# Kernel optimization log

Hardware: AMD Instinct MI355X
Metric: run time of the kernel (lower is better)

## Reference

```python
import jax, jax.numpy as jnp
import numpy as np

H, L, OUT = 128, 3, 128
N, E, NRG, ERG, M, G = 200_000, 600_000, 100_000, 300_000, 200_000, 10_000
BN_EPS = 1e-5


def setup_inputs() -> dict:
    key = jax.random.key(0)
    ks = iter(jax.random.split(key, 32))
    rint = lambda shape, hi: jax.random.randint(next(ks), shape, 0, hi, dtype=jnp.int64 if False else jnp.int32)
    inp = {
        "node_feat": rint((N, 9), 100),
        "edge_index": rint((2, E), N),
        "edge_feat": rint((E, 3), 100),
        "batch": jnp.sort(rint((N,), G)),
        "mapping_row": rint((M,), N),
        "mapping_col": rint((M,), NRG),
        "rg_edge_index": rint((2, ERG), NRG),
        "rg_atom_features": rint((NRG,), 8),
        "tree_batch": jnp.sort(rint((NRG,), G)),
        "num_graphs": G,
    }
    s = 0.05
    nrm = lambda shape: jax.random.normal(next(ks), shape, dtype=jnp.float32) * s
    inp.update({
        "atom_emb": nrm((9, 100, H)),
        "bond_emb": nrm((L, 3, 100, H)),
        "rg_emb": nrm((8, H)),
        "atom_W1": nrm((L, H, 2 * H)),
        "atom_W2": nrm((L, 2 * H, H)),
        "rg_W1": nrm((L, H, 2 * H)),
        "rg_W2": nrm((L, 2 * H, H)),
        "raw2rg_W": nrm((L, H, H)),
        "rg2raw_W": nrm((L, H, H)),
        "atom_lin_W": nrm((H, H)),
        "rg_lin_W": nrm((H, H)),
        "lin_W": nrm((H, OUT)),
    })
    return inp


def _scatter_mean(src, idx, n):
    s = jax.ops.segment_sum(src, idx, num_segments=n)
    c = jax.ops.segment_sum(jnp.ones((src.shape[0], 1), src.dtype), idx, num_segments=n)
    return s / jnp.maximum(c, 1.0)


def _bn(h):  # BatchNorm1d(affine=False), batch statistics
    mu = h.mean(0)
    var = h.var(0)
    return (h - mu) * jax.lax.rsqrt(var + BN_EPS)


def _gin_mlp(h, W1, W2):  # Linear -> BN -> ReLU -> Linear (all bias-free)
    return jax.nn.relu(_bn(h @ W1)) @ W2


def reference(node_feat, edge_index, edge_feat, batch, mapping_row, mapping_col,
              rg_edge_index, rg_atom_features, tree_batch, num_graphs,
              atom_emb, bond_emb, rg_emb, atom_W1, atom_W2, rg_W1, rg_W2,
              raw2rg_W, rg2raw_W, atom_lin_W, rg_lin_W, lin_W):
    n = node_feat.shape[0]
    n_rg = rg_atom_features.shape[0]
    src, dst = edge_index[0], edge_index[1]
    rsrc, rdst = rg_edge_index[0], rg_edge_index[1]

    # AtomEncoder: sum of 9 embedding lookups -> [n, H]
    x = atom_emb[jnp.arange(9), node_feat].sum(axis=1)
    rg = rg_emb[rg_atom_features]  # [n_rg, H]

    for i in range(L):
        # BondEncoder + GINEConv: sum_j relu(x_j + e_ij) aggregated at dst
        e = bond_emb[i][jnp.arange(3), edge_feat].sum(axis=1)  # [E, H]
        agg = jax.ops.segment_sum(jax.nn.relu(x[src] + e), dst, num_segments=n)
        x = jax.nn.relu(_bn(_gin_mlp(x + agg, atom_W1[i], atom_W2[i])))

        # raw -> reduced-graph inter message passing (scatter mean over mapping)
        rg = rg + jax.nn.relu(_scatter_mean(x[mapping_row], mapping_col, n_rg) @ raw2rg_W[i])

        # GINConv on reduced graph
        agg_rg = jax.ops.segment_sum(rg[rsrc], rdst, num_segments=n_rg)
        rg = jax.nn.relu(_bn(_gin_mlp(rg + agg_rg, rg_W1[i], rg_W2[i])))

        # reduced-graph -> raw inter message passing
        x = x + jax.nn.relu(_scatter_mean(rg[mapping_col], mapping_row, n) @ rg2raw_W[i])

    # graph-level readout (mean pooling)
    xg = _scatter_mean(x, batch, num_graphs) @ atom_lin_W
    rgg = _scatter_mean(rg, tree_batch, num_graphs) @ rg_lin_W
    return jax.nn.relu(xg + rgg) @ lin_W  # [num_graphs, OUT]
```

## Files before the change

kernel.cpp:

```cpp
#include <hip/hip_runtime.h>
#include <hip/hip_bf16.h>
#include <cstdint>
#include <cstddef>

#define H 128

using f32x4v = __attribute__((ext_vector_type(4))) float;
using bf8 = __attribute__((ext_vector_type(8))) short;

__device__ __forceinline__ short f2bf(float f) {
  unsigned u = __float_as_uint(f);
  u = (u + 0x7fffu + ((u >> 16) & 1u)) >> 16;
  return (short)u;
}
__device__ __forceinline__ float bf2f(short h) {
  return __uint_as_float(((unsigned)(unsigned short)h) << 16);
}
__device__ __forceinline__ void splitf(float f, short& h, short& l) {
  h = f2bf(f);
  l = f2bf(f - bf2f(h));
}
__device__ __forceinline__ f32x4v mfma16(bf8 a, bf8 b, f32x4v c) {
  return __builtin_amdgcn_mfma_f32_16x16x32_bf16(a, b, c, 0, 0, 0);
}

__device__ __forceinline__ void load_afrags(const float* __restrict__ Ap, bool av,
    float sc, bf8* ah, bf8* al_) {
#pragma unroll
  for (int ks = 0; ks < 4; ++ks) {
    float v[8];
    if (av) {
      f32x4v p0 = *(const f32x4v*)(Ap + ks * 32);
      f32x4v p1 = *(const f32x4v*)(Ap + ks * 32 + 4);
      v[0]=p0.x*sc; v[1]=p0.y*sc; v[2]=p0.z*sc; v[3]=p0.w*sc;
      v[4]=p1.x*sc; v[5]=p1.y*sc; v[6]=p1.z*sc; v[7]=p1.w*sc;
    } else {
#pragma unroll
      for (int j = 0; j < 8; ++j) v[j] = 0.f;
    }
#pragma unroll
    for (int j = 0; j < 8; ++j) { short hh, ll; splitf(v[j], hh, ll); ah[ks][j]=hh; al_[ks][j]=ll; }
  }
}


__global__ __launch_bounds__(256) void pack_w_k(const float* __restrict__ W,
    short* __restrict__ hi, short* __restrict__ lo, int K, int N) {
  int total = K * N;
  int t = blockIdx.x * 256 + threadIdx.x;
  int layer = blockIdx.y;
  if (t >= total) return;
  int k = t / N, n = t - k * N;
  float f = W[(size_t)layer * total + t];
  short h, l; splitf(f, h, l);
  int nt = n >> 4, ks = k >> 5, kk = k & 31;
  int lane = (n & 15) | (((kk >> 3) & 3) << 4);
  size_t idx = (size_t)layer * total + ((size_t)(nt * (K >> 5) + ks) << 9) + lane * 8 + (kk & 7);
  hi[idx] = h; lo[idx] = l;
}


__global__ __launch_bounds__(256) void atom_encode_k(const int* __restrict__ nf,
    const float* __restrict__ emb, float* __restrict__ x, int N) {
  long long t = (long long)blockIdx.x * 256 + threadIdx.x;
  if (t >= (long long)N * H) return;
  int n = (int)(t >> 7), h = (int)(t & 127);
  const int* row = nf + (size_t)n * 9;
  float s = 0.f;
#pragma unroll
  for (int f = 0; f < 9; ++f) s += emb[((size_t)f * 100 + row[f]) * H + h];
  x[t] = s;
}

__global__ __launch_bounds__(256) void rg_init_k(const int* __restrict__ feat,
    const float* __restrict__ emb, float* __restrict__ rg, int NRG) {
  long long t = (long long)blockIdx.x * 256 + threadIdx.x;
  if (t >= (long long)NRG * H) return;
  int n = (int)(t >> 7), h = (int)(t & 127);
  rg[t] = emb[(size_t)feat[n] * H + h];
}


__global__ __launch_bounds__(256) void icount_k(const int* __restrict__ idx,
    int* __restrict__ cnt, int n) {
  int t = blockIdx.x * 256 + threadIdx.x;
  if (t < n) atomicAdd(&cnt[idx[t]], 1);
}

__global__ __launch_bounds__(256) void inv_from_int_k(const int* __restrict__ c,
    float* __restrict__ inv, int n) {
  int t = blockIdx.x * 256 + threadIdx.x;
  if (t < n) inv[t] = 1.0f / (float)max(c[t], 1);
}

__global__ __launch_bounds__(256) void seg_blocksum_k(const int* __restrict__ cnt,
    int* __restrict__ bsum, int n) {
  __shared__ int red[256];
  int base = blockIdx.x * 1024;
  int s = 0;
  for (int i = threadIdx.x; i < 1024; i += 256) {
    int idx = base + i;
    s += (idx < n) ? cnt[idx] : 0;
  }
  red[threadIdx.x] = s; __syncthreads();
  for (int st = 128; st > 0; st >>= 1) {
    if (threadIdx.x < st) red[threadIdx.x] += red[threadIdx.x + st];
    __syncthreads();
  }
  if (threadIdx.x == 0) bsum[blockIdx.x] = red[0];
}

__global__ __launch_bounds__(256) void seg_scan_k(const int* __restrict__ cnt,
    const int* __restrict__ bsum, int* __restrict__ off, int* __restrict__ cur,
    int n, int nblk) {
  __shared__ int pref;
  __shared__ int tsum[257];
  int b = blockIdx.x;
  if (threadIdx.x == 0) {
    int p = 0;
    for (int j = 0; j < b; ++j) p += bsum[j];
    pref = p;
  }
  int base = b * 1024 + threadIdx.x * 4;
  int v[4]; int s = 0;
#pragma unroll
  for (int j = 0; j < 4; ++j) { int idx = base + j; v[j] = (idx < n) ? cnt[idx] : 0; s += v[j]; }
  tsum[threadIdx.x + 1] = s;
  if (threadIdx.x == 0) tsum[0] = 0;
  __syncthreads();
  if (threadIdx.x == 0) { for (int j = 1; j <= 256; ++j) tsum[j] += tsum[j - 1]; }
  __syncthreads();
  int run = pref + tsum[threadIdx.x];
#pragma unroll
  for (int j = 0; j < 4; ++j) {
    int idx = base + j;
    if (idx < n) { off[idx] = run; cur[idx] = run; }
    run += v[j];
  }
  if (b == 0 && threadIdx.x == 0) {
    int tot = 0;
    for (int j = 0; j < nblk; ++j) tot += bsum[j];
    off[n] = tot;
  }
}

__global__ __launch_bounds__(256) void seg_fill_k(const int* __restrict__ idx,
    int* __restrict__ cur, int* __restrict__ ids, int n) {
  int t = blockIdx.x * 256 + threadIdx.x;
  if (t < n) { int p = atomicAdd(&cur[idx[t]], 1); ids[p] = t; }
}


__global__ __launch_bounds__(256) void gine_agg_k(const int* __restrict__ off,
    const int* __restrict__ ids, const int* __restrict__ ei, const int* __restrict__ ef,
    const float* __restrict__ bemb, const float* __restrict__ x,
    float* __restrict__ out, int N) {
  int n = blockIdx.x * 8 + (threadIdx.x >> 5);
  if (n >= N) return;
  int c4 = (threadIdx.x & 31) * 4;
  float4 acc = *(const float4*)(x + (size_t)n * H + c4);
  int p0 = off[n], p1 = off[n + 1];
  for (int p = p0; p < p1; ++p) {
    int e = ids[p];
    int src = ei[e];
    const int* f = ef + (size_t)e * 3;
    float4 v0 = *(const float4*)(bemb + (size_t)f[0] * H + c4);
    float4 v1 = *(const float4*)(bemb + ((size_t)100 + f[1]) * H + c4);
    float4 v2 = *(const float4*)(bemb + ((size_t)200 + f[2]) * H + c4);
    float4 xs = *(const float4*)(x + (size_t)src * H + c4);
    acc.x += fmaxf(xs.x + v0.x + v1.x + v2.x, 0.f);
    acc.y += fmaxf(xs.y + v0.y + v1.y + v2.y, 0.f);
    acc.z += fmaxf(xs.z + v0.z + v1.z + v2.z, 0.f);
    acc.w += fmaxf(xs.w + v0.w + v1.w + v2.w, 0.f);
  }
  *(float4*)(out + (size_t)n * H + c4) = acc;
}

__global__ __launch_bounds__(256) void gather_agg_k(const int* __restrict__ off,
    const int* __restrict__ ids, const int* __restrict__ sidx,
    const float* __restrict__ src, const float* __restrict__ base,
    float* __restrict__ out, int N) {
  int n = blockIdx.x * 8 + (threadIdx.x >> 5);
  if (n >= N) return;
  int c4 = (threadIdx.x & 31) * 4;
  float4 acc = make_float4(0.f, 0.f, 0.f, 0.f);
  if (base) acc = *(const float4*)(base + (size_t)n * H + c4);
  int p0 = off[n], p1 = off[n + 1];
  for (int p = p0; p < p1; ++p) {
    int m = ids[p];
    int sr = sidx ? sidx[m] : m;
    float4 v = *(const float4*)(src + (size_t)sr * H + c4);
    acc.x += v.x; acc.y += v.y; acc.z += v.z; acc.w += v.w;
  }
  *(float4*)(out + (size_t)n * H + c4) = acc;
}

__device__ __forceinline__ int lowb(const int* __restrict__ a, int n, int v) {
  int lo = 0, hi = n;
  while (lo < hi) { int mid = (lo + hi) >> 1; if (a[mid] < v) lo = mid + 1; else hi = mid; }
  return lo;
}

__global__ __launch_bounds__(256) void pool_mean_k(const int* __restrict__ bidx,
    const float* __restrict__ src, float* __restrict__ out, int n, int G) {
  int g = blockIdx.x * 8 + (threadIdx.x >> 5);
  if (g >= G) return;
  int c4 = (threadIdx.x & 31) * 4;
  int lo = lowb(bidx, n, g), hi = lowb(bidx, n, g + 1);
  float4 acc = make_float4(0.f, 0.f, 0.f, 0.f);
  for (int r = lo; r < hi; ++r) {
    float4 v = *(const float4*)(src + (size_t)r * H + c4);
    acc.x += v.x; acc.y += v.y; acc.z += v.z; acc.w += v.w;
  }
  float inv = 1.0f / (float)max(hi - lo, 1);
  acc.x *= inv; acc.y *= inv; acc.z *= inv; acc.w *= inv;
  *(float4*)(out + (size_t)g * H + c4) = acc;
}


__global__ void bn_final_k(const float* __restrict__ ssum, const float* __restrict__ ssq,
    float* __restrict__ mu, float* __restrict__ rsig, int C, float invM) {
  int c = threadIdx.x + blockIdx.x * blockDim.x;
  if (c < C) {
    float m = ssum[c] * invM;
    float v = ssq[c] * invM - m * m;
    mu[c] = m;
    rsig[c] = rsqrtf(v + 1e-5f);
  }
}

__global__ __launch_bounds__(256) void bn_apply_relu_k(const float* __restrict__ X,
    const float* __restrict__ mu, const float* __restrict__ rsig,
    float* __restrict__ Out, int M) {
  long long t = (long long)blockIdx.x * 256 + threadIdx.x;
  if (t >= (long long)M * 32) return;
  int c4 = ((int)(t & 31)) * 4;
  float4 v = ((const float4*)X)[t];
  float4 m4 = *(const float4*)&mu[c4];
  float4 r4 = *(const float4*)&rsig[c4];
  v.x = fmaxf((v.x - m4.x) * r4.x, 0.f);
  v.y = fmaxf((v.y - m4.y) * r4.y, 0.f);
  v.z = fmaxf((v.z - m4.z) * r4.z, 0.f);
  v.w = fmaxf((v.w - m4.w) * r4.w, 0.f);
  ((float4*)Out)[t] = v;
}


__global__ __launch_bounds__(512) void mlp_stats_mfma_k(
    const float* __restrict__ A, const short* __restrict__ w1h, const short* __restrict__ w1l,
    float* __restrict__ ssum, float* __restrict__ ssq, int M, int npairs) {
  __shared__ __align__(16) short Wch[8192], Wcl[8192];
  __shared__ float sRed[256], qRed[256];
  int tid = threadIdx.x;
  if (tid < 256) { sRed[tid] = 0.f; qRed[tid] = 0.f; }
  int w = tid >> 6, l = tid & 63, l15 = l & 15, lg = l >> 4;
  int h = w >> 2, wl = w & 3;
  float sAcc[16], qAcc[16];
#pragma unroll
  for (int nt = 0; nt < 16; ++nt) { sAcc[nt] = 0.f; qAcc[nt] = 0.f; }
  for (int pb = blockIdx.x; pb < npairs; pb += gridDim.x) {
    int tile = pb * 2 + h;
    int arow = tile * 64 + wl * 16 + l15;
    bool av = arow < M;
    bf8 ah[4], al_[4];
    load_afrags(A + (size_t)arow * 128 + lg * 8, av, 1.f, ah, al_);
    for (int ch = 0; ch < 4; ++ch) {
      __syncthreads();
      const bf8* srcH = (const bf8*)(w1h + ch * 8192);
      const bf8* srcL = (const bf8*)(w1l + ch * 8192);
      for (int it = tid; it < 1024; it += 512) {
        ((bf8*)Wch)[it] = srcH[it];
        ((bf8*)Wcl)[it] = srcL[it];
      }
      __syncthreads();
#pragma unroll
      for (int ntl = 0; ntl < 4; ++ntl) {
        f32x4v c = {0.f, 0.f, 0.f, 0.f};
#pragma unroll
        for (int ks = 0; ks < 4; ++ks) {
          bf8 bh = *(const bf8*)&Wch[(ntl * 4 + ks) * 512 + l * 8];
          bf8 bl = *(const bf8*)&Wcl[(ntl * 4 + ks) * 512 + l * 8];
          c = mfma16(al_[ks], bh, c);
          c = mfma16(ah[ks], bl, c);
          c = mfma16(ah[ks], bh, c);
        }
        int nt = ch * 4 + ntl;
        if (av) {
          sAcc[nt] += c[0] + c[1] + c[2] + c[3];
          qAcc[nt] += c[0]*c[0] + c[1]*c[1] + c[2]*c[2] + c[3]*c[3];
        }
      }
    }
  }
  __syncthreads();
#pragma unroll
  for (int nt = 0; nt < 16; ++nt) {
    float s = sAcc[nt], q = qAcc[nt];
    s += __shfl_xor(s, 16); s += __shfl_xor(s, 32);
    q += __shfl_xor(q, 16); q += __shfl_xor(q, 32);
    if (l < 16) { atomicAdd(&sRed[nt * 16 + l], s); atomicAdd(&qRed[nt * 16 + l], q); }
  }
  __syncthreads();
  if (tid < 256) { atomicAdd(&ssum[tid], sRed[tid]); atomicAdd(&ssq[tid], qRed[tid]); }
}



__global__ __launch_bounds__(512) void mlp_fused_mfma_k(
    float* __restrict__ A, const short* __restrict__ w1h, const short* __restrict__ w1l,
    const short* __restrict__ w2h, const short* __restrict__ w2l,
    const float* __restrict__ mu, const float* __restrict__ rsig,
    float* __restrict__ ssum, float* __restrict__ ssq, int M, int npairs) {
  __shared__ __align__(16) short Wch[8192], Wcl[8192];
  __shared__ __align__(16) float h1f[2][64][132];
  __shared__ float sRed[128], qRed[128];
  int tid = threadIdx.x;
  if (tid < 128) { sRed[tid] = 0.f; qRed[tid] = 0.f; }
  int w = tid >> 6, l = tid & 63, l15 = l & 15, lg = l >> 4;
  int h = w >> 2, wl = w & 3;
  float sAcc[8], qAcc[8];
#pragma unroll
  for (int nt = 0; nt < 8; ++nt) { sAcc[nt] = 0.f; qAcc[nt] = 0.f; }
  for (int pb = blockIdx.x; pb < npairs; pb += gridDim.x) {
    int tile = pb * 2 + h;
    int arow = tile * 64 + wl * 16 + l15;
    bool av = arow < M;
    f32x4v acc[8];
#pragma unroll
    for (int nt = 0; nt < 8; ++nt) acc[nt] = (f32x4v){0.f, 0.f, 0.f, 0.f};
    for (int kh = 0; kh < 2; ++kh) {
      {
        bf8 ah[4], al_[4];
        load_afrags(A + (size_t)arow * 128 + lg * 8, av, 1.f, ah, al_);
        for (int ch = 0; ch < 2; ++ch) {
          int cbase = kh * 8 + ch * 4;
          __syncthreads();
          const bf8* srcH = (const bf8*)(w1h + cbase * 2048);
          const bf8* srcL = (const bf8*)(w1l + cbase * 2048);
          for (int it = tid; it < 1024; it += 512) {
            ((bf8*)Wch)[it] = srcH[it];
            ((bf8*)Wcl)[it] = srcL[it];
          }
          __syncthreads();
#pragma unroll
          for (int ntl = 0; ntl < 4; ++ntl) {
            f32x4v c = {0.f, 0.f, 0.f, 0.f};
#pragma unroll
            for (int ks = 0; ks < 4; ++ks) {
              bf8 bh = *(const bf8*)&Wch[(ntl * 4 + ks) * 512 + l * 8];
              bf8 bl = *(const bf8*)&Wcl[(ntl * 4 + ks) * 512 + l * 8];
              c = mfma16(al_[ks], bh, c);
              c = mfma16(ah[ks], bl, c);
              c = mfma16(ah[ks], bh, c);
            }
            int cn = cbase + ntl;
            int cc = cn * 16 + l15;
            float mm = mu[cc], rs = rsig[cc];
#pragma unroll
            for (int r = 0; r < 4; ++r) {
              float t = fmaxf((c[r] - mm) * rs, 0.f);
              h1f[h][wl * 16 + lg * 4 + r][(cn & 7) * 16 + l15] = t;
            }
          }
        }
      }
      __syncthreads();
      bf8 a2h[4], a2l[4];
#pragma unroll
      for (int ks2 = 0; ks2 < 4; ++ks2) {
        const float* hp = &h1f[h][wl * 16 + l15][ks2 * 32 + lg * 8];
#pragma unroll
        for (int j = 0; j < 8; ++j) {
          short hh, ll; splitf(hp[j], hh, ll);
          a2h[ks2][j] = hh; a2l[ks2][j] = ll;
        }
      }
      for (int c2 = 0; c2 < 2; ++c2) {
        __syncthreads();
        for (int it = tid; it < 1024; it += 512) {
          int e = it * 8;
          int ntl = e >> 11, rem = e & 2047;
          int ks2 = rem >> 9, s = rem & 511;
          int src = ((c2 * 4 + ntl) * 8 + kh * 4 + ks2) * 512 + s;
          ((bf8*)Wch)[it] = *(const bf8*)(w2h + src);
          ((bf8*)Wcl)[it] = *(const bf8*)(w2l + src);
        }
        __syncthreads();
#pragma unroll
        for (int ntl = 0; ntl < 4; ++ntl) {
          f32x4v c = acc[c2 * 4 + ntl];
#pragma unroll
          for (int ks2 = 0; ks2 < 4; ++ks2) {
            bf8 bh = *(const bf8*)&Wch[(ntl * 4 + ks2) * 512 + l * 8];
            bf8 bl = *(const bf8*)&Wcl[(ntl * 4 + ks2) * 512 + l * 8];
            c = mfma16(a2l[ks2], bh, c);
            c = mfma16(a2h[ks2], bl, c);
            c = mfma16(a2h[ks2], bh, c);
          }
          acc[c2 * 4 + ntl] = c;
        }
      }
    }
    int base = tile * 64 + wl * 16;
#pragma unroll
    for (int nt = 0; nt < 8; ++nt) {
      int cc = nt * 16 + l15;
#pragma unroll
      for (int r = 0; r < 4; ++r) {
        int gr = base + lg * 4 + r;
        if (gr < M) {
          float vv = acc[nt][r];
          A[(size_t)gr * 128 + cc] = vv;
          sAcc[nt] += vv;
          qAcc[nt] = fmaf(vv, vv, qAcc[nt]);
        }
      }
    }
  }
  __syncthreads();
#pragma unroll
  for (int nt = 0; nt < 8; ++nt) {
    float s = sAcc[nt], q = qAcc[nt];
    s += __shfl_xor(s, 16); s += __shfl_xor(s, 32);
    q += __shfl_xor(q, 16); q += __shfl_xor(q, 32);
    if (l < 16) { atomicAdd(&sRed[nt * 16 + l], s); atomicAdd(&qRed[nt * 16 + l], q); }
  }
  __syncthreads();
  if (tid < 128) { atomicAdd(&ssum[tid], sRed[tid]); atomicAdd(&ssq[tid], qRed[tid]); }
}


__global__ __launch_bounds__(256) void gemm128_mfma_k(
    const float* __restrict__ A0, const float* __restrict__ AUX,
    const short* __restrict__ wh, const short* __restrict__ wl,
    float* __restrict__ Out, int M, int ntiles) {
  __shared__ __align__(16) short Wh[16384], Wl[16384];
  int tid = threadIdx.x;
  for (int i = tid; i < 2048; i += 256) {
    ((f32x4v*)Wh)[i] = ((const f32x4v*)wh)[i];
    ((f32x4v*)Wl)[i] = ((const f32x4v*)wl)[i];
  }
  __syncthreads();
  int w = tid >> 6, l = tid & 63, l15 = l & 15, lg = l >> 4;
  for (int tb = blockIdx.x; tb < ntiles; tb += gridDim.x) {
    int arow = tb * 64 + w * 16 + l15;
    bool av = arow < M;
    float sc = av ? AUX[arow] : 0.f;
    bf8 ah[4], al_[4];
    load_afrags(A0 + (size_t)arow * 128 + lg * 8, av, sc, ah, al_);
    int base = tb * 64 + w * 16;
#pragma unroll
    for (int nt = 0; nt < 8; ++nt) {
      f32x4v c = {0.f, 0.f, 0.f, 0.f};
#pragma unroll
      for (int ks = 0; ks < 4; ++ks) {
        bf8 bh = *(const bf8*)&Wh[(nt * 4 + ks) * 512 + l * 8];
        bf8 bl = *(const bf8*)&Wl[(nt * 4 + ks) * 512 + l * 8];
        c = mfma16(al_[ks], bh, c);
        c = mfma16(ah[ks], bl, c);
        c = mfma16(ah[ks], bh, c);
      }
#pragma unroll
      for (int r = 0; r < 4; ++r) {
        int gr = base + lg * 4 + r;
        if (gr < M) {
          size_t o = (size_t)gr * 128 + nt * 16 + l15;
          Out[o] = Out[o] + fmaxf(c[r], 0.f);
        }
      }
    }
  }
}

template<int EPI>
__global__ __launch_bounds__(256) void gemm_k(
    const float* __restrict__ A0, const float* __restrict__ W,
    float* __restrict__ Out, int M) {
  __shared__ __align__(16) float Ash[64][64];
  int tid = threadIdx.x;
  int tc = tid & 63, tr = tid >> 6;
  int row0 = blockIdx.x * 64;
  float acc[16][2];
#pragma unroll
  for (int i = 0; i < 16; ++i) { acc[i][0] = 0.f; acc[i][1] = 0.f; }
  for (int k0 = 0; k0 < 128; k0 += 64) {
#pragma unroll
    for (int it = 0; it < 4; ++it) {
      int fidx = tid + it * 256;
      int r = fidx >> 4, c4 = (fidx & 15) << 2;
      int gr = row0 + r;
      float4 v = make_float4(0.f, 0.f, 0.f, 0.f);
      if (gr < M) v = *(const float4*)(A0 + (size_t)gr * 128 + k0 + c4);
      *(float4*)&Ash[r][c4] = v;
    }
    __syncthreads();
    const float* Wp = W + (size_t)k0 * 128 + tc;
    for (int kk = 0; kk < 64; kk += 4) {
      float w[4][2];
#pragma unroll
      for (int kj = 0; kj < 4; ++kj)
#pragma unroll
        for (int j = 0; j < 2; ++j) w[kj][j] = Wp[(size_t)(kk + kj) * 128 + j * 64];
#pragma unroll
      for (int i = 0; i < 16; ++i) {
        float4 a = *(const float4*)&Ash[tr * 16 + i][kk];
#pragma unroll
        for (int j = 0; j < 2; ++j) {
          acc[i][j] = fmaf(a.x, w[0][j], acc[i][j]);
          acc[i][j] = fmaf(a.y, w[1][j], acc[i][j]);
          acc[i][j] = fmaf(a.z, w[2][j], acc[i][j]);
          acc[i][j] = fmaf(a.w, w[3][j], acc[i][j]);
        }
      }
    }
    __syncthreads();
  }
#pragma unroll
  for (int i = 0; i < 16; ++i) {
    int gr = row0 + tr * 16 + i;
    if (gr < M) {
#pragma unroll
      for (int j = 0; j < 2; ++j) {
        size_t o = (size_t)gr * 128 + tc + j * 64;
        float v = acc[i][j];
        if (EPI == 0) Out[o] = v;
        else Out[o] = fmaxf(Out[o] + v, 0.f);
      }
    }
  }
}


static inline int cdivll(long long a, long long b) { return (int)((a + b - 1) / b); }

extern "C" void kernel_launch(void* const* d_in, const int* in_sizes, int n_in,
                              void* d_out, int out_size, void* d_ws, size_t ws_size,
                              hipStream_t stream) {
  const int* node_feat  = (const int*)d_in[0];
  const int* edge_index = (const int*)d_in[1];
  const int* edge_feat  = (const int*)d_in[2];
  const int* batch      = (const int*)d_in[3];
  const int* map_row    = (const int*)d_in[4];
  const int* map_col    = (const int*)d_in[5];
  const int* rg_ei      = (const int*)d_in[6];
  const int* rg_feat    = (const int*)d_in[7];
  const int* tree_batch = (const int*)d_in[8];
  const float* atom_emb   = (const float*)d_in[10];
  const float* bond_emb   = (const float*)d_in[11];
  const float* rg_emb     = (const float*)d_in[12];
  const float* atom_W1    = (const float*)d_in[13];
  const float* atom_W2    = (const float*)d_in[14];
  const float* rg_W1      = (const float*)d_in[15];
  const float* rg_W2      = (const float*)d_in[16];
  const float* raw2rg_W   = (const float*)d_in[17];
  const float* rg2raw_W   = (const float*)d_in[18];
  const float* atom_lin_W = (const float*)d_in[19];
  const float* rg_lin_W   = (const float*)d_in[20];
  const float* lin_W      = (const float*)d_in[21];

  const int N   = in_sizes[0] / 9;
  const int E   = in_sizes[1] / 2;
  const int M   = in_sizes[4];
  const int NRG = in_sizes[7];
  const int ERG = in_sizes[6] / 2;
  const int G   = out_size / H;
  if (N <= 0 || G <= 0) return;

  const size_t NH = (size_t)N * H, RH = (size_t)NRG * H, GH = (size_t)G * H;
  const int cmax = max(N, NRG);

  const size_t nfloat = 2 * NH + RH + (size_t)NRG + (size_t)N + 1024;
  const size_t nint = (size_t)(N + 1) * 2 + (size_t)(NRG + 1) * 2
                    + (size_t)E + 2 * (size_t)M + (size_t)ERG + (size_t)cmax + 1024;
  const size_t nshort = 3 * (4 * 32768 + 2 * 16384);
  const size_t need = nfloat * 4 + nint * 4 + nshort * 2 + 256;
  if (ws_size < need) return;

  float* ws = (float*)d_ws;
  size_t off = 0;
  auto alloc = [&](size_t n) { float* p = ws + off; off += n; return p; };
  float* x       = alloc(NH);
  float* abuf    = alloc(NH);
  float* rg      = alloc(RH);
  float* inv_col = alloc((size_t)NRG);
  float* inv_row = alloc((size_t)N);
  float* ssum = alloc(256);
  float* ssq  = alloc(256);
  float* mu   = alloc(256);
  float* rsig = alloc(256);

  int* ip = (int*)(ws + off);
  size_t ioff = 0;
  auto ialloc = [&](size_t n) { int* p = ip + ioff; ioff += n; return p; };
  int* off_dst = ialloc((size_t)N + 1);
  int* off_col = ialloc((size_t)NRG + 1);
  int* off_row = ialloc((size_t)N + 1);
  int* off_rg  = ialloc((size_t)NRG + 1);
  int* ids_dst = ialloc((size_t)E);
  int* ids_col = ialloc((size_t)M);
  int* ids_row = ialloc((size_t)M);
  int* ids_rg  = ialloc((size_t)ERG);
  int* tmp_cnt = ialloc((size_t)cmax);
  int* bsum    = ialloc(1024);

  short* sp = (short*)(ip + ioff);
  size_t soff = 0;
  auto salloc = [&](size_t n) { short* p = sp + soff; soff += n; return p; };
  short* paW1h = salloc(3 * 32768); short* paW1l = salloc(3 * 32768);
  short* paW2h = salloc(3 * 32768); short* paW2l = salloc(3 * 32768);
  short* prW1h = salloc(3 * 32768); short* prW1l = salloc(3 * 32768);
  short* prW2h = salloc(3 * 32768); short* prW2l = salloc(3 * 32768);
  short* p2gh  = salloc(3 * 16384); short* p2gl  = salloc(3 * 16384);
  short* pg2h  = salloc(3 * 16384); short* pg2l  = salloc(3 * 16384);

  const int ta = (N + 63) >> 6, trg = (NRG + 63) >> 6;
  const int pa = (ta + 1) >> 1, prg = (trg + 1) >> 1;
  const int ga2 = pa < 512 ? pa : 512, grg2 = prg < 512 ? prg : 512;
  const int ga = ta < 512 ? ta : 512, grg = trg < 512 ? trg : 512;

  pack_w_k<<<dim3(128, 3), 256, 0, stream>>>(atom_W1, paW1h, paW1l, 128, 256);
  pack_w_k<<<dim3(128, 3), 256, 0, stream>>>(atom_W2, paW2h, paW2l, 256, 128);
  pack_w_k<<<dim3(128, 3), 256, 0, stream>>>(rg_W1, prW1h, prW1l, 128, 256);
  pack_w_k<<<dim3(128, 3), 256, 0, stream>>>(rg_W2, prW2h, prW2l, 256, 128);
  pack_w_k<<<dim3(64, 3), 256, 0, stream>>>(raw2rg_W, p2gh, p2gl, 128, 128);
  pack_w_k<<<dim3(64, 3), 256, 0, stream>>>(rg2raw_W, pg2h, pg2l, 128, 128);

  auto build_csr = [&](const int* idx, int nelem, int nrows, int* offs, int* ids,
                       float* inv) {
    hipMemsetAsync(tmp_cnt, 0, (size_t)nrows * 4, stream);
    icount_k<<<cdivll(nelem, 256), 256, 0, stream>>>(idx, tmp_cnt, nelem);
    if (inv) inv_from_int_k<<<cdivll(nrows, 256), 256, 0, stream>>>(tmp_cnt, inv, nrows);
    int nblk = cdivll(nrows, 1024);
    seg_blocksum_k<<<nblk, 256, 0, stream>>>(tmp_cnt, bsum, nrows);
    seg_scan_k<<<nblk, 256, 0, stream>>>(tmp_cnt, bsum, offs, tmp_cnt, nrows, nblk);
    seg_fill_k<<<cdivll(nelem, 256), 256, 0, stream>>>(idx, tmp_cnt, ids, nelem);
  };
  build_csr(edge_index + E, E, N, off_dst, ids_dst, nullptr);
  build_csr(map_col, M, NRG, off_col, ids_col, inv_col);
  build_csr(map_row, M, N, off_row, ids_row, inv_row);
  build_csr(rg_ei + ERG, ERG, NRG, off_rg, ids_rg, nullptr);

  atom_encode_k<<<cdivll(NH, 256), 256, 0, stream>>>(node_feat, atom_emb, x, N);
  rg_init_k<<<cdivll(RH, 256), 256, 0, stream>>>(rg_feat, rg_emb, rg, NRG);

  for (int i = 0; i < 3; ++i) {
    gine_agg_k<<<cdivll(N, 8), 256, 0, stream>>>(off_dst, ids_dst, edge_index, edge_feat,
        bond_emb + (size_t)i * 3 * 100 * H, x, abuf, N);
    hipMemsetAsync(ssum, 0, 512 * 4, stream);
    mlp_stats_mfma_k<<<ga2, 512, 0, stream>>>(abuf, paW1h + i * 32768, paW1l + i * 32768, ssum, ssq, N, pa);
    bn_final_k<<<1, 256, 0, stream>>>(ssum, ssq, mu, rsig, 256, 1.0f / N);
    hipMemsetAsync(ssum, 0, 512 * 4, stream);
    mlp_fused_mfma_k<<<ga2, 512, 0, stream>>>(abuf, paW1h + i * 32768, paW1l + i * 32768,
        paW2h + i * 32768, paW2l + i * 32768, mu, rsig, ssum, ssq, N, pa);
    bn_final_k<<<1, 256, 0, stream>>>(ssum, ssq, mu, rsig, 128, 1.0f / N);
    bn_apply_relu_k<<<cdivll((long long)N * 32, 256), 256, 0, stream>>>(abuf, mu, rsig, x, N);

    gather_agg_k<<<cdivll(NRG, 8), 256, 0, stream>>>(off_col, ids_col, map_row, x, nullptr, abuf, NRG);
    gemm128_mfma_k<<<grg, 256, 0, stream>>>(abuf, inv_col, p2gh + i * 16384, p2gl + i * 16384,
        rg, NRG, trg);

    gather_agg_k<<<cdivll(NRG, 8), 256, 0, stream>>>(off_rg, ids_rg, rg_ei, rg, rg, abuf, NRG);
    hipMemsetAsync(ssum, 0, 512 * 4, stream);
    mlp_stats_mfma_k<<<grg2, 512, 0, stream>>>(abuf, prW1h + i * 32768, prW1l + i * 32768, ssum, ssq, NRG, prg);
    bn_final_k<<<1, 256, 0, stream>>>(ssum, ssq, mu, rsig, 256, 1.0f / NRG);
    hipMemsetAsync(ssum, 0, 512 * 4, stream);
    mlp_fused_mfma_k<<<grg2, 512, 0, stream>>>(abuf, prW1h + i * 32768, prW1l + i * 32768,
        prW2h + i * 32768, prW2l + i * 32768, mu, rsig, ssum, ssq, NRG, prg);
    bn_final_k<<<1, 256, 0, stream>>>(ssum, ssq, mu, rsig, 128, 1.0f / NRG);
    bn_apply_relu_k<<<cdivll((long long)NRG * 32, 256), 256, 0, stream>>>(abuf, mu, rsig, rg, NRG);

    gather_agg_k<<<cdivll(N, 8), 256, 0, stream>>>(off_row, ids_row, map_col, rg, nullptr, abuf, N);
    gemm128_mfma_k<<<ga, 256, 0, stream>>>(abuf, inv_row, pg2h + i * 16384, pg2l + i * 16384,
        x, N, ta);
  }

  float* xg  = abuf;
  float* rgg = abuf + GH;
  float* P   = abuf + 2 * GH;
  pool_mean_k<<<cdivll(G, 8), 256, 0, stream>>>(batch, x, xg, N, G);
  pool_mean_k<<<cdivll(G, 8), 256, 0, stream>>>(tree_batch, rg, rgg, NRG, G);
  gemm_k<0><<<cdivll(G, 64), 256, 0, stream>>>(xg, atom_lin_W, P, G);
  gemm_k<2><<<cdivll(G, 64), 256, 0, stream>>>(rgg, rg_lin_W, P, G);
  gemm_k<0><<<cdivll(G, 64), 256, 0, stream>>>(P, lin_W, (float*)d_out, G);
}
```

Measured before the change: 3.198 ms.

## Compute first BatchNorm stats from Gram matrix; fuse mapping gather into GEMM

The first BN statistics pass no longer runs the full A@W1 GEMM. It computes the Gram matrix A^T A and the column sums of A with split-bf16 MFMA, using x and rg as scratch for per-block partials. Small kernels then derive the mean and variance of A@W1 as W1^T sA and diag(W1^T G W1). Separately, the scatter-mean gather for the inter-graph message passing is fused into the 128-wide GEMM kernel, so the aggregate no longer goes through abuf. This removes GEMM work and a round trip through global memory. The cost is variance computed as E[y^2]-mu^2 from a Gram reduction, which is less numerically stable, plus extra small serial kernels.

```diff
diff --git a/kernel.cpp b/kernel.cpp
--- a/kernel.cpp
+++ b/kernel.cpp
@@ -4,6 +4,7 @@
 #include <cstddef>
 
 #define H 128
+#define GNB 256
 
 using f32x4v = __attribute__((ext_vector_type(4))) float;
 using bf8 = __attribute__((ext_vector_type(8))) short;
@@ -246,64 +247,115 @@
 }
 
 
-__global__ __launch_bounds__(512) void mlp_stats_mfma_k(
-    const float* __restrict__ A, const short* __restrict__ w1h, const short* __restrict__ w1l,
-    float* __restrict__ ssum, float* __restrict__ ssq, int M, int npairs) {
-  __shared__ __align__(16) short Wch[8192], Wcl[8192];
-  __shared__ float sRed[256], qRed[256];
+#define GT(t, CI, CJ) \
+  acc[t] = mfma16(fl[CI], fh[CJ], acc[t]); \
+  acc[t] = mfma16(fh[CI], fl[CJ], acc[t]); \
+  acc[t] = mfma16(fh[CI], fh[CJ], acc[t]);
+
+#define GW(t, CI, CJ) \
+  { Gp[((CI)*16 + lg*4 + 0) * 128 + (CJ)*16 + l15] = acc[t][0]; \
+    Gp[((CI)*16 + lg*4 + 1) * 128 + (CJ)*16 + l15] = acc[t][1]; \
+    Gp[((CI)*16 + lg*4 + 2) * 128 + (CJ)*16 + l15] = acc[t][2]; \
+    Gp[((CI)*16 + lg*4 + 3) * 128 + (CJ)*16 + l15] = acc[t][3]; }
+
+__global__ __launch_bounds__(256) void gram_k(const float* __restrict__ A,
+    float* __restrict__ Gpart, float* __restrict__ sApart, int M, int ntiles) {
   int tid = threadIdx.x;
-  if (tid < 256) { sRed[tid] = 0.f; qRed[tid] = 0.f; }
   int w = tid >> 6, l = tid & 63, l15 = l & 15, lg = l >> 4;
-  int h = w >> 2, wl = w & 3;
-  float sAcc[16], qAcc[16];
-#pragma unroll
-  for (int nt = 0; nt < 16; ++nt) { sAcc[nt] = 0.f; qAcc[nt] = 0.f; }
-  for (int pb = blockIdx.x; pb < npairs; pb += gridDim.x) {
-    int tile = pb * 2 + h;
-    int arow = tile * 64 + wl * 16 + l15;
-    bool av = arow < M;
-    bf8 ah[4], al_[4];
-    load_afrags(A + (size_t)arow * 128 + lg * 8, av, 1.f, ah, al_);
-    for (int ch = 0; ch < 4; ++ch) {
-      __syncthreads();
-      const bf8* srcH = (const bf8*)(w1h + ch * 8192);
-      const bf8* srcL = (const bf8*)(w1l + ch * 8192);
-      for (int it = tid; it < 1024; it += 512) {
-        ((bf8*)Wch)[it] = srcH[it];
-        ((bf8*)Wcl)[it] = srcL[it];
-      }
-      __syncthreads();
-#pragma unroll
-      for (int ntl = 0; ntl < 4; ++ntl) {
-        f32x4v c = {0.f, 0.f, 0.f, 0.f};
-#pragma unroll
-        for (int ks = 0; ks < 4; ++ks) {
-          bf8 bh = *(const bf8*)&Wch[(ntl * 4 + ks) * 512 + l * 8];
-          bf8 bl = *(const bf8*)&Wcl[(ntl * 4 + ks) * 512 + l * 8];
-          c = mfma16(al_[ks], bh, c);
-          c = mfma16(ah[ks], bl, c);
-          c = mfma16(ah[ks], bh, c);
-        }
-        int nt = ch * 4 + ntl;
-        if (av) {
-          sAcc[nt] += c[0] + c[1] + c[2] + c[3];
-          qAcc[nt] += c[0]*c[0] + c[1]*c[1] + c[2]*c[2] + c[3]*c[3];
-        }
-      }
-    }
-  }
-  __syncthreads();
-#pragma unroll
-  for (int nt = 0; nt < 16; ++nt) {
-    float s = sAcc[nt], q = qAcc[nt];
-    s += __shfl_xor(s, 16); s += __shfl_xor(s, 32);
-    q += __shfl_xor(q, 16); q += __shfl_xor(q, 32);
-    if (l < 16) { atomicAdd(&sRed[nt * 16 + l], s); atomicAdd(&qRed[nt * 16 + l], q); }
-  }
-  __syncthreads();
-  if (tid < 256) { atomicAdd(&ssum[tid], sRed[tid]); atomicAdd(&ssq[tid], qRed[tid]); }
-}
-
+  f32x4v acc[9];
+#pragma unroll
+  for (int t = 0; t < 9; ++t) acc[t] = (f32x4v){0.f, 0.f, 0.f, 0.f};
+  float sAcol[8];
+#pragma unroll
+  for (int c = 0; c < 8; ++c) sAcol[c] = 0.f;
+  for (int tb = blockIdx.x; tb < ntiles; tb += GNB) {
+    int rb = tb * 64;
+#pragma unroll
+    for (int ks = 0; ks < 2; ++ks) {
+      bf8 fh[8], fl[8];
+      int rowb = rb + ks * 32 + lg * 8;
+#pragma unroll
+      for (int c = 0; c < 8; ++c) {
+#pragma unroll
+        for (int j = 0; j < 8; ++j) {
+          int gr = rowb + j;
+          float v = (gr < M) ? A[(size_t)gr * 128 + c * 16 + l15] : 0.f;
+          if (w == 0) sAcol[c] += v;
+          short hh, ll; splitf(v, hh, ll);
+          fh[c][j] = hh; fl[c][j] = ll;
+        }
+      }
+      if (w == 0) {
+        GT(0,0,0) GT(1,0,1) GT(2,0,2) GT(3,0,3) GT(4,0,4) GT(5,0,5) GT(6,0,6) GT(7,0,7) GT(8,7,7)
+      } else if (w == 1) {
+        GT(0,1,1) GT(1,1,2) GT(2,1,3) GT(3,1,4) GT(4,1,5) GT(5,1,6) GT(6,1,7) GT(7,6,6) GT(8,6,7)
+      } else if (w == 2) {
+        GT(0,2,2) GT(1,2,3) GT(2,2,4) GT(3,2,5) GT(4,2,6) GT(5,2,7) GT(6,5,5) GT(7,5,6) GT(8,5,7)
+      } else {
+        GT(0,3,3) GT(1,3,4) GT(2,3,5) GT(3,3,6) GT(4,3,7) GT(5,4,4) GT(6,4,5) GT(7,4,6) GT(8,4,7)
+      }
+    }
+  }
+  float* Gp = Gpart + (size_t)blockIdx.x * 16384;
+  if (w == 0) {
+    GW(0,0,0) GW(1,0,1) GW(2,0,2) GW(3,0,3) GW(4,0,4) GW(5,0,5) GW(6,0,6) GW(7,0,7) GW(8,7,7)
+#pragma unroll
+    for (int c = 0; c < 8; ++c) {
+      float s = sAcol[c];
+      s += __shfl_xor(s, 16); s += __shfl_xor(s, 32);
+      if (l < 16) sApart[(size_t)blockIdx.x * 128 + c * 16 + l] = s;
+    }
+  } else if (w == 1) {
+    GW(0,1,1) GW(1,1,2) GW(2,1,3) GW(3,1,4) GW(4,1,5) GW(5,1,6) GW(6,1,7) GW(7,6,6) GW(8,6,7)
+  } else if (w == 2) {
+    GW(0,2,2) GW(1,2,3) GW(2,2,4) GW(3,2,5) GW(4,2,6) GW(5,2,7) GW(6,5,5) GW(7,5,6) GW(8,5,7)
+  } else {
+    GW(0,3,3) GW(1,3,4) GW(2,3,5) GW(3,3,6) GW(4,3,7) GW(5,4,4) GW(6,4,5) GW(7,4,6) GW(8,4,7)
+  }
+}
+
+__global__ __launch_bounds__(256) void gram_reduce_k(const float* __restrict__ Gpart,
+    const float* __restrict__ sApart, float* __restrict__ G, float* __restrict__ sA) {
+  int t = blockIdx.x * 256 + threadIdx.x;
+  int i = t >> 7, j = t & 127;
+  if (i <= j) {
+    float s = 0.f;
+    for (int b = 0; b < GNB; ++b) s += Gpart[(size_t)b * 16384 + t];
+    G[t] = s;
+    G[j * 128 + i] = s;
+  }
+  if (t < 128) {
+    float s = 0.f;
+    for (int b = 0; b < GNB; ++b) s += sApart[(size_t)b * 128 + t];
+    sA[t] = s;
+  }
+}
+
+__global__ __launch_bounds__(256) void gemmy_k(const float* __restrict__ G,
+    const float* __restrict__ W1, float* __restrict__ y) {
+  int i = blockIdx.x, c = threadIdx.x;
+  const float* Gi = G + i * 128;
+  float acc = 0.f;
+#pragma unroll 4
+  for (int j = 0; j < 128; ++j) acc += Gi[j] * W1[j * 256 + c];
+  y[i * 256 + c] = acc;
+}
+
+__global__ __launch_bounds__(256) void bn1fin_k(const float* __restrict__ sA,
+    const float* __restrict__ y, const float* __restrict__ W1,
+    float* __restrict__ mu, float* __restrict__ rsig, float invM) {
+  int c = threadIdx.x;
+  float m = 0.f, ev = 0.f;
+#pragma unroll 4
+  for (int i = 0; i < 128; ++i) {
+    float w1 = W1[i * 256 + c];
+    m += sA[i] * w1;
+    ev += w1 * y[i * 256 + c];
+  }
+  m *= invM; ev *= invM;
+  mu[c] = m;
+  rsig[c] = rsqrtf(ev - m * m + 1e-5f);
+}
 
 
 __global__ __launch_bounds__(512) void mlp_fused_mfma_k(
@@ -430,8 +482,10 @@
 }
 
 
-__global__ __launch_bounds__(256) void gemm128_mfma_k(
-    const float* __restrict__ A0, const float* __restrict__ AUX,
+__global__ __launch_bounds__(256) void gemm128g_k(
+    const int* __restrict__ off, const int* __restrict__ ids,
+    const int* __restrict__ sidx, const float* __restrict__ src,
+    const float* __restrict__ inv,
     const short* __restrict__ wh, const short* __restrict__ wl,
     float* __restrict__ Out, int M, int ntiles) {
   __shared__ __align__(16) short Wh[16384], Wl[16384];
@@ -445,9 +499,35 @@
   for (int tb = blockIdx.x; tb < ntiles; tb += gridDim.x) {
     int arow = tb * 64 + w * 16 + l15;
     bool av = arow < M;
-    float sc = av ? AUX[arow] : 0.f;
+    float g[4][8];
+#pragma unroll
+    for (int ks = 0; ks < 4; ++ks)
+#pragma unroll
+      for (int j = 0; j < 8; ++j) g[ks][j] = 0.f;
+    if (av) {
+      int p0 = off[arow], p1 = off[arow + 1];
+      for (int p = p0; p < p1; ++p) {
+        int m = ids[p];
+        int sr = sidx ? sidx[m] : m;
+        const float* S = src + (size_t)sr * 128 + lg * 8;
+#pragma unroll
+        for (int ks = 0; ks < 4; ++ks) {
+          f32x4v a = *(const f32x4v*)(S + ks * 32);
+          f32x4v b = *(const f32x4v*)(S + ks * 32 + 4);
+          g[ks][0] += a.x; g[ks][1] += a.y; g[ks][2] += a.z; g[ks][3] += a.w;
+          g[ks][4] += b.x; g[ks][5] += b.y; g[ks][6] += b.z; g[ks][7] += b.w;
+        }
+      }
+    }
+    float sc = av ? inv[arow] : 0.f;
     bf8 ah[4], al_[4];
-    load_afrags(A0 + (size_t)arow * 128 + lg * 8, av, sc, ah, al_);
+#pragma unroll
+    for (int ks = 0; ks < 4; ++ks)
+#pragma unroll
+      for (int j = 0; j < 8; ++j) {
+        short hh, ll; splitf(g[ks][j] * sc, hh, ll);
+        ah[ks][j] = hh; al_[ks][j] = ll;
+      }
     int base = tb * 64 + w * 16;
 #pragma unroll
     for (int nt = 0; nt < 8; ++nt) {
@@ -568,13 +648,16 @@
 
   const size_t NH = (size_t)N * H, RH = (size_t)NRG * H, GH = (size_t)G * H;
   const int cmax = max(N, NRG);
-
-  const size_t nfloat = 2 * NH + RH + (size_t)NRG + (size_t)N + 1024;
+  const size_t gram_sz = (size_t)GNB * 16384 + (size_t)GNB * 128;
+
+  const size_t nfloat = 2 * NH + RH + (size_t)NRG + (size_t)N
+                      + 16384 + 128 + 32768 + 1024;
   const size_t nint = (size_t)(N + 1) * 2 + (size_t)(NRG + 1) * 2
                     + (size_t)E + 2 * (size_t)M + (size_t)ERG + (size_t)cmax + 1024;
   const size_t nshort = 3 * (4 * 32768 + 2 * 16384);
   const size_t need = nfloat * 4 + nint * 4 + nshort * 2 + 256;
   if (ws_size < need) return;
+  if (RH < gram_sz || NH < gram_sz) return;
 
   float* ws = (float*)d_ws;
   size_t off = 0;
@@ -584,10 +667,16 @@
   float* rg      = alloc(RH);
   float* inv_col = alloc((size_t)NRG);
   float* inv_row = alloc((size_t)N);
+  float* Gm      = alloc(16384);
+  float* sA      = alloc(128);
+  float* ybuf    = alloc(32768);
   float* ssum = alloc(256);
   float* ssq  = alloc(256);
   float* mu   = alloc(256);
   float* rsig = alloc(256);
+
+  float* GpartA = x;   float* sApartA = x + (size_t)GNB * 16384;
+  float* GpartR = rg;  float* sApartR = rg + (size_t)GNB * 16384;
 
   int* ip = (int*)(ws + off);
   size_t ioff = 0;
@@ -644,34 +733,37 @@
   rg_init_k<<<cdivll(RH, 256), 256, 0, stream>>>(rg_feat, rg_emb, rg, NRG);
 
   for (int i = 0; i < 3; ++i) {
+    const float* aW1f = atom_W1 + (size_t)i * 32768;
+    const float* rW1f = rg_W1 + (size_t)i * 32768;
+
     gine_agg_k<<<cdivll(N, 8), 256, 0, stream>>>(off_dst, ids_dst, edge_index, edge_feat,
         bond_emb + (size_t)i * 3 * 100 * H, x, abuf, N);
-    hipMemsetAsync(ssum, 0, 512 * 4, stream);
-    mlp_stats_mfma_k<<<ga2, 512, 0, stream>>>(abuf, paW1h + i * 32768, paW1l + i * 32768, ssum, ssq, N, pa);
-    bn_final_k<<<1, 256, 0, stream>>>(ssum, ssq, mu, rsig, 256, 1.0f / N);
+    gram_k<<<GNB, 256, 0, stream>>>(abuf, GpartA, sApartA, N, ta);
+    gram_reduce_k<<<64, 256, 0, stream>>>(GpartA, sApartA, Gm, sA);
+    gemmy_k<<<128, 256, 0, stream>>>(Gm, aW1f, ybuf);
+    bn1fin_k<<<1, 256, 0, stream>>>(sA, ybuf, aW1f, mu, rsig, 1.0f / N);
     hipMemsetAsync(ssum, 0, 512 * 4, stream);
     mlp_fused_mfma_k<<<ga2, 512, 0, stream>>>(abuf, paW1h + i * 32768, paW1l + i * 32768,
         paW2h + i * 32768, paW2l + i * 32768, mu, rsig, ssum, ssq, N, pa);
     bn_final_k<<<1, 256, 0, stream>>>(ssum, ssq, mu, rsig, 128, 1.0f / N);
     bn_apply_relu_k<<<cdivll((long long)N * 32, 256), 256, 0, stream>>>(abuf, mu, rsig, x, N);
 
-    gather_agg_k<<<cdivll(NRG, 8), 256, 0, stream>>>(off_col, ids_col, map_row, x, nullptr, abuf, NRG);
-    gemm128_mfma_k<<<grg, 256, 0, stream>>>(abuf, inv_col, p2gh + i * 16384, p2gl + i * 16384,
-        rg, NRG, trg);
+    gemm128g_k<<<grg, 256, 0, stream>>>(off_col, ids_col, map_row, x, inv_col,
+        p2gh + i * 16384, p2gl + i * 16384, rg, NRG, trg);
 
     gather_agg_k<<<cdivll(NRG, 8), 256, 0, stream>>>(off_rg, ids_rg, rg_ei, rg, rg, abuf, NRG);
-    hipMemsetAsync(ssum, 0, 512 * 4, stream);
-    mlp_stats_mfma_k<<<grg2, 512, 0, stream>>>(abuf, prW1h + i * 32768, prW1l + i * 32768, ssum, ssq, NRG, prg);
-    bn_final_k<<<1, 256, 0, stream>>>(ssum, ssq, mu, rsig, 256, 1.0f / NRG);
+    gram_k<<<GNB, 256, 0, stream>>>(abuf, GpartR, sApartR, NRG, trg);
+    gram_reduce_k<<<64, 256, 0, stream>>>(GpartR, sApartR, Gm, sA);
+    gemmy_k<<<128, 256, 0, stream>>>(Gm, rW1f, ybuf);
+    bn1fin_k<<<1, 256, 0, stream>>>(sA, ybuf, rW1f, mu, rsig, 1.0f / NRG);
     hipMemsetAsync(ssum, 0, 512 * 4, stream);
     mlp_fused_mfma_k<<<grg2, 512, 0, stream>>>(abuf, prW1h + i * 32768, prW1l + i * 32768,
         prW2h + i * 32768, prW2l + i * 32768, mu, rsig, ssum, ssq, NRG, prg);
     bn_final_k<<<1, 256, 0, stream>>>(ssum, ssq, mu, rsig, 128, 1.0f / NRG);
     bn_apply_relu_k<<<cdivll((long long)NRG * 32, 256), 256, 0, stream>>>(abuf, mu, rsig, rg, NRG);
 
-    gather_agg_k<<<cdivll(N, 8), 256, 0, stream>>>(off_row, ids_row, map_col, rg, nullptr, abuf, N);
-    gemm128_mfma_k<<<ga, 256, 0, stream>>>(abuf, inv_row, pg2h + i * 16384, pg2l + i * 16384,
-        x, N, ta);
+    gemm128g_k<<<ga, 256, 0, stream>>>(off_row, ids_row, map_col, rg, inv_row,
+        pg2h + i * 16384, pg2l + i * 16384, x, N, ta);
   }
 
   float* xg  = abuf;
```

New measurement: 3.626 ms. 13.4% more time.

## Unroll gather loops by two and restructure fused MLP into four K-chunks

Applied to the files above, without the earlier changes.

The GINE and plain gather-aggregation loops now process two edges per iteration into two accumulators, so more independent loads are in flight. The fused MLP kernel is restructured from two K halves into four 64-wide chunks. Each chunk computes 64 hidden columns, stores them in a smaller LDS buffer, and immediately accumulates their contribution through W2. This shrinks LDS use for h1f, which may allow more blocks per CU. In exchange the A fragments are reloaded from global memory four times instead of twice, and the number of barriers changes. The workspace float reserve is also slightly enlarged.

```diff
diff --git a/kernel.cpp b/kernel.cpp
--- a/kernel.cpp
+++ b/kernel.cpp
@@ -159,8 +159,32 @@
   if (n >= N) return;
   int c4 = (threadIdx.x & 31) * 4;
   float4 acc = *(const float4*)(x + (size_t)n * H + c4);
+  float4 acc2 = make_float4(0.f, 0.f, 0.f, 0.f);
   int p0 = off[n], p1 = off[n + 1];
-  for (int p = p0; p < p1; ++p) {
+  int p = p0;
+  for (; p + 1 < p1; p += 2) {
+    int e0 = ids[p], e1 = ids[p + 1];
+    int s0 = ei[e0], s1 = ei[e1];
+    const int* f0 = ef + (size_t)e0 * 3;
+    const int* f1 = ef + (size_t)e1 * 3;
+    float4 a0 = *(const float4*)(bemb + (size_t)f0[0] * H + c4);
+    float4 a1 = *(const float4*)(bemb + ((size_t)100 + f0[1]) * H + c4);
+    float4 a2 = *(const float4*)(bemb + ((size_t)200 + f0[2]) * H + c4);
+    float4 xa = *(const float4*)(x + (size_t)s0 * H + c4);
+    float4 b0 = *(const float4*)(bemb + (size_t)f1[0] * H + c4);
+    float4 b1 = *(const float4*)(bemb + ((size_t)100 + f1[1]) * H + c4);
+    float4 b2 = *(const float4*)(bemb + ((size_t)200 + f1[2]) * H + c4);
+    float4 xb = *(const float4*)(x + (size_t)s1 * H + c4);
+    acc.x += fmaxf(xa.x + a0.x + a1.x + a2.x, 0.f);
+    acc.y += fmaxf(xa.y + a0.y + a1.y + a2.y, 0.f);
+    acc.z += fmaxf(xa.z + a0.z + a1.z + a2.z, 0.f);
+    acc.w += fmaxf(xa.w + a0.w + a1.w + a2.w, 0.f);
+    acc2.x += fmaxf(xb.x + b0.x + b1.x + b2.x, 0.f);
+    acc2.y += fmaxf(xb.y + b0.y + b1.y + b2.y, 0.f);
+    acc2.z += fmaxf(xb.z + b0.z + b1.z + b2.z, 0.f);
+    acc2.w += fmaxf(xb.w + b0.w + b1.w + b2.w, 0.f);
+  }
+  if (p < p1) {
     int e = ids[p];
     int src = ei[e];
     const int* f = ef + (size_t)e * 3;
@@ -173,6 +197,7 @@
     acc.z += fmaxf(xs.z + v0.z + v1.z + v2.z, 0.f);
     acc.w += fmaxf(xs.w + v0.w + v1.w + v2.w, 0.f);
   }
+  acc.x += acc2.x; acc.y += acc2.y; acc.z += acc2.z; acc.w += acc2.w;
   *(float4*)(out + (size_t)n * H + c4) = acc;
 }
 
@@ -184,14 +209,26 @@
   if (n >= N) return;
   int c4 = (threadIdx.x & 31) * 4;
   float4 acc = make_float4(0.f, 0.f, 0.f, 0.f);
+  float4 acc2 = make_float4(0.f, 0.f, 0.f, 0.f);
   if (base) acc = *(const float4*)(base + (size_t)n * H + c4);
   int p0 = off[n], p1 = off[n + 1];
-  for (int p = p0; p < p1; ++p) {
+  int p = p0;
+  for (; p + 1 < p1; p += 2) {
+    int m0 = ids[p], m1 = ids[p + 1];
+    int s0 = sidx ? sidx[m0] : m0;
+    int s1 = sidx ? sidx[m1] : m1;
+    float4 v0 = *(const float4*)(src + (size_t)s0 * H + c4);
+    float4 v1 = *(const float4*)(src + (size_t)s1 * H + c4);
+    acc.x += v0.x; acc.y += v0.y; acc.z += v0.z; acc.w += v0.w;
+    acc2.x += v1.x; acc2.y += v1.y; acc2.z += v1.z; acc2.w += v1.w;
+  }
+  if (p < p1) {
     int m = ids[p];
     int sr = sidx ? sidx[m] : m;
     float4 v = *(const float4*)(src + (size_t)sr * H + c4);
     acc.x += v.x; acc.y += v.y; acc.z += v.z; acc.w += v.w;
   }
+  acc.x += acc2.x; acc.y += acc2.y; acc.z += acc2.z; acc.w += acc2.w;
   *(float4*)(out + (size_t)n * H + c4) = acc;
 }
 
@@ -305,14 +342,13 @@
 }
 
 
-
 __global__ __launch_bounds__(512) void mlp_fused_mfma_k(
     float* __restrict__ A, const short* __restrict__ w1h, const short* __restrict__ w1l,
     const short* __restrict__ w2h, const short* __restrict__ w2l,
     const float* __restrict__ mu, const float* __restrict__ rsig,
     float* __restrict__ ssum, float* __restrict__ ssq, int M, int npairs) {
   __shared__ __align__(16) short Wch[8192], Wcl[8192];
-  __shared__ __align__(16) float h1f[2][64][132];
+  __shared__ __align__(16) float h1f[2][64][68];
   __shared__ float sRed[128], qRed[128];
   int tid = threadIdx.x;
   if (tid < 128) { sRed[tid] = 0.f; qRed[tid] = 0.f; }
@@ -328,46 +364,52 @@
     f32x4v acc[8];
 #pragma unroll
     for (int nt = 0; nt < 8; ++nt) acc[nt] = (f32x4v){0.f, 0.f, 0.f, 0.f};
-    for (int kh = 0; kh < 2; ++kh) {
+    for (int kq = 0; kq < 4; ++kq) {
+      bf8 ah[4], al_[4];
+      load_afrags(A + (size_t)arow * 128 + lg * 8, av, 1.f, ah, al_);
+      __syncthreads();
       {
-        bf8 ah[4], al_[4];
-        load_afrags(A + (size_t)arow * 128 + lg * 8, av, 1.f, ah, al_);
-        for (int ch = 0; ch < 2; ++ch) {
-          int cbase = kh * 8 + ch * 4;
-          __syncthreads();
-          const bf8* srcH = (const bf8*)(w1h + cbase * 2048);
-          const bf8* srcL = (const bf8*)(w1l + cbase * 2048);
-          for (int it = tid; it < 1024; it += 512) {
-            ((bf8*)Wch)[it] = srcH[it];
-            ((bf8*)Wcl)[it] = srcL[it];
-          }
-          __syncthreads();
-#pragma unroll
-          for (int ntl = 0; ntl < 4; ++ntl) {
-            f32x4v c = {0.f, 0.f, 0.f, 0.f};
-#pragma unroll
-            for (int ks = 0; ks < 4; ++ks) {
-              bf8 bh = *(const bf8*)&Wch[(ntl * 4 + ks) * 512 + l * 8];
-              bf8 bl = *(const bf8*)&Wcl[(ntl * 4 + ks) * 512 + l * 8];
-              c = mfma16(al_[ks], bh, c);
-              c = mfma16(ah[ks], bl, c);
-              c = mfma16(ah[ks], bh, c);
-            }
-            int cn = cbase + ntl;
-            int cc = cn * 16 + l15;
-            float mm = mu[cc], rs = rsig[cc];
-#pragma unroll
-            for (int r = 0; r < 4; ++r) {
-              float t = fmaxf((c[r] - mm) * rs, 0.f);
-              h1f[h][wl * 16 + lg * 4 + r][(cn & 7) * 16 + l15] = t;
-            }
-          }
+        const bf8* srcH = (const bf8*)(w1h + kq * 8192);
+        const bf8* srcL = (const bf8*)(w1l + kq * 8192);
+        for (int it = tid; it < 1024; it += 512) {
+          ((bf8*)Wch)[it] = srcH[it];
+          ((bf8*)Wcl)[it] = srcL[it];
         }
       }
       __syncthreads();
-      bf8 a2h[4], a2l[4];
-#pragma unroll
-      for (int ks2 = 0; ks2 < 4; ++ks2) {
+#pragma unroll
+      for (int ntl = 0; ntl < 4; ++ntl) {
+        f32x4v c = {0.f, 0.f, 0.f, 0.f};
+#pragma unroll
+        for (int ks = 0; ks < 4; ++ks) {
+          bf8 bh = *(const bf8*)&Wch[(ntl * 4 + ks) * 512 + l * 8];
+          bf8 bl = *(const bf8*)&Wcl[(ntl * 4 + ks) * 512 + l * 8];
+          c = mfma16(al_[ks], bh, c);
+          c = mfma16(ah[ks], bl, c);
+          c = mfma16(ah[ks], bh, c);
+        }
+        int cc = (kq * 4 + ntl) * 16 + l15;
+        float mm = mu[cc], rs = rsig[cc];
+#pragma unroll
+        for (int r = 0; r < 4; ++r) {
+          float t = fmaxf((c[r] - mm) * rs, 0.f);
+          h1f[h][wl * 16 + lg * 4 + r][ntl * 16 + l15] = t;
+        }
+      }
+      __syncthreads();
+      {
+        for (int it = tid; it < 1024; it += 512) {
+          int nt2 = it >> 7, rem = it & 127;
+          int ks2l = rem >> 6, s8 = rem & 63;
+          int srcb = (nt2 * 8 + kq * 2 + ks2l) * 64 + s8;
+          ((bf8*)Wch)[it] = ((const bf8*)w2h)[srcb];
+          ((bf8*)Wcl)[it] = ((const bf8*)w2l)[srcb];
+        }
+      }
+      __syncthreads();
+      bf8 a2h[2], a2l[2];
+#pragma unroll
+      for (int ks2 = 0; ks2 < 2; ++ks2) {
         const float* hp = &h1f[h][wl * 16 + l15][ks2 * 32 + lg * 8];
 #pragma unroll
         for (int j = 0; j < 8; ++j) {
@@ -375,30 +417,18 @@
           a2h[ks2][j] = hh; a2l[ks2][j] = ll;
         }
       }
-      for (int c2 = 0; c2 < 2; ++c2) {
-        __syncthreads();
-        for (int it = tid; it < 1024; it += 512) {
-          int e = it * 8;
-          int ntl = e >> 11, rem = e & 2047;
-          int ks2 = rem >> 9, s = rem & 511;
-          int src = ((c2 * 4 + ntl) * 8 + kh * 4 + ks2) * 512 + s;
-          ((bf8*)Wch)[it] = *(const bf8*)(w2h + src);
-          ((bf8*)Wcl)[it] = *(const bf8*)(w2l + src);
-        }
-        __syncthreads();
-#pragma unroll
-        for (int ntl = 0; ntl < 4; ++ntl) {
-          f32x4v c = acc[c2 * 4 + ntl];
-#pragma unroll
-          for (int ks2 = 0; ks2 < 4; ++ks2) {
-            bf8 bh = *(const bf8*)&Wch[(ntl * 4 + ks2) * 512 + l * 8];
-            bf8 bl = *(const bf8*)&Wcl[(ntl * 4 + ks2) * 512 + l * 8];
-            c = mfma16(a2l[ks2], bh, c);
-            c = mfma16(a2h[ks2], bl, c);
-            c = mfma16(a2h[ks2], bh, c);
-          }
-          acc[c2 * 4 + ntl] = c;
-        }
+#pragma unroll
+      for (int nt = 0; nt < 8; ++nt) {
+        f32x4v c = acc[nt];
+#pragma unroll
+        for (int ks2 = 0; ks2 < 2; ++ks2) {
+          bf8 bh = *(const bf8*)&Wch[(nt * 2 + ks2) * 512 + l * 8];
+          bf8 bl = *(const bf8*)&Wcl[(nt * 2 + ks2) * 512 + l * 8];
+          c = mfma16(a2l[ks2], bh, c);
+          c = mfma16(a2h[ks2], bl, c);
+          c = mfma16(a2h[ks2], bh, c);
+        }
+        acc[nt] = c;
       }
     }
     int base = tile * 64 + wl * 16;
@@ -569,7 +599,7 @@
   const size_t NH = (size_t)N * H, RH = (size_t)NRG * H, GH = (size_t)G * H;
   const int cmax = max(N, NRG);
 
-  const size_t nfloat = 2 * NH + RH + (size_t)NRG + (size_t)N + 1024;
+  const size_t nfloat = 2 * NH + RH + (size_t)NRG + (size_t)N + 2048;
   const size_t nint = (size_t)(N + 1) * 2 + (size_t)(NRG + 1) * 2
                     + (size_t)E + 2 * (size_t)M + (size_t)ERG + (size_t)cmax + 1024;
   const size_t nshort = 3 * (4 * 32768 + 2 * 16384);
```

After: 3.243 ms. About the same (+1.4%).
